# Performance work log

Hardware: AMD Instinct MI355X
Metric: run time of the kernel (lower is better)

## Reference

```python
import jax, jax.numpy as jnp
import numpy as np

P_FACTOR = 3.0
EPS = 1e-12  # torch F.normalize eps


def _l2norm(x):
    # torch.nn.functional.normalize(x, dim=1): x / max(||x||_2, eps)
    n = jnp.sqrt(jnp.sum(x * x, axis=1, keepdims=True))
    return x / jnp.maximum(n, EPS)


def setup_inputs() -> dict:
    key = jax.random.key(0)
    k1, k2, k3, k4, k5 = jax.random.split(key, 5)
    B, N, D_IN, D_RED, C = 8192, 16384, 1024, 512, 28
    return {
        "features": jax.random.normal(k1, (B, D_IN), dtype=jnp.float32),
        "ex_features": jax.random.normal(k2, (N, D_IN), dtype=jnp.float32),
        "g_w": jax.random.normal(k3, (D_RED, D_IN), dtype=jnp.float32) * 0.02,
        "g_b": jax.random.normal(k4, (D_RED,), dtype=jnp.float32) * 0.02,
        "ex_classes": jax.random.uniform(k5, (N, C), dtype=jnp.float32),
    }


def reference(features, ex_features, g_w, g_b, ex_classes):
    # g: Linear(input_dim -> dim_reduce)
    f = features @ g_w.T + g_b          # [B, D_red]
    ef = ex_features @ g_w.T + g_b      # [N, D_red]
    # cosine similarity
    s = _l2norm(f) @ _l2norm(ef).T      # [B, N]
    # power-sign activation: |s|^p * sign(s)
    a = jnp.power(jnp.abs(s), P_FACTOR) * jnp.sign(s)
    echo = a @ ex_classes               # [B, C]
    b = jnp.clip(jnp.sum(ex_classes, axis=0), 1.0, None)
    echo = jnp.clip(echo / b, 0.0, 1.0)
    return echo
```

## Files before the change

kernel.cpp:

```cpp
#include <hip/hip_runtime.h>
#include <stdint.h>

typedef __attribute__((ext_vector_type(4))) float f32x4;
typedef __attribute__((ext_vector_type(8))) short s16x8;

#define MFMA16(A, B, C) __builtin_amdgcn_mfma_f32_16x16x32_bf16(A, B, C, 0, 0, 0)
#define WAIT_VM(N) asm volatile("s_waitcnt vmcnt(" #N ")" ::: "memory")
#define WAIT_LGKM() asm volatile("s_waitcnt lgkmcnt(0)" ::: "memory")
#define BAR() __builtin_amdgcn_s_barrier()
#define SCHED_FENCE() __builtin_amdgcn_sched_barrier(0)
#define SP1() __builtin_amdgcn_s_setprio(1)
#define SP0() __builtin_amdgcn_s_setprio(0)

__device__ __forceinline__ unsigned short f2bf(float x) {
  union { float f; unsigned u; } v; v.f = x;
  return (unsigned short)((v.u + 0x7fffu + ((v.u >> 16) & 1u)) >> 16);
}

__global__ void k_cast_bf16(const float* __restrict__ in, unsigned short* __restrict__ out, int n4) {
  int i = blockIdx.x * blockDim.x + threadIdx.x;
  const int stride = gridDim.x * blockDim.x;
  for (; i < n4; i += stride) {
    const float4 v = ((const float4*)in)[i];
    ushort4 o;
    o.x = f2bf(v.x); o.y = f2bf(v.y); o.z = f2bf(v.z); o.w = f2bf(v.w);
    ((ushort4*)out)[i] = o;
  }
}

__global__ void k_excT(const float* __restrict__ exc, unsigned short* __restrict__ excT,
                       float* __restrict__ bvec) {
  const int c = blockIdx.x;
  const int tid = threadIdx.x;
  float sum = 0.f;
  for (int j = tid; j < 16384; j += 256) {
    const float v = (c < 28) ? exc[(size_t)j * 28 + c] : 0.f;
    excT[(size_t)c * 16384 + j] = f2bf(v);
    sum += v;
  }
  #pragma unroll
  for (int o = 32; o; o >>= 1) sum += __shfl_down(sum, o, 64);
  __shared__ float wsum[4];
  if ((tid & 63) == 0) wsum[tid >> 6] = sum;
  __syncthreads();
  if (tid == 0 && c < 28) bvec[c] = fmaxf(wsum[0] + wsum[1] + wsum[2] + wsum[3], 1.0f);
}

__device__ __forceinline__ void stage_a(const unsigned short* __restrict__ src, int ld,
                                        unsigned short* smem, int dsoff, int w, int offsrc) {
  #pragma unroll
  for (int c = 0; c < 4; ++c)
    __builtin_amdgcn_global_load_lds(
        (const __attribute__((address_space(1))) unsigned int*)(src + offsrc + c * 64 * ld),
        (__attribute__((address_space(3))) unsigned int*)(smem + dsoff + c * 4096 + w * 512),
        16, 0, 0);
}
__device__ __forceinline__ void stage_b(const unsigned short* __restrict__ src, int ld,
                                        unsigned short* smem, int dsoff, int w, int offsrc) {
  #pragma unroll
  for (int c = 0; c < 2; ++c)
    __builtin_amdgcn_global_load_lds(
        (const __attribute__((address_space(1))) unsigned int*)(src + offsrc + c * 64 * ld),
        (__attribute__((address_space(3))) unsigned int*)(smem + dsoff + c * 4096 + w * 512),
        16, 0, 0);
}

__device__ __forceinline__ void mma_step_p(const unsigned short* smem, int ao, int bo,
                                           int wr, int wc, int r, int q, f32x4 acc[8][2]) {
  const int rx = r & 7;
  #pragma unroll
  for (int ks = 0; ks < 2; ++ks) {
    const int sb = ((ks * 4 + q) ^ rx) << 3;
    s16x8 bf[2];
    #pragma unroll
    for (int j = 0; j < 2; ++j)
      bf[j] = *(const s16x8*)(smem + bo + (wc * 32 + j * 16 + r) * 64 + sb);
    #pragma unroll
    for (int i = 0; i < 8; ++i) {
      const s16x8 af = *(const s16x8*)(smem + ao + (wr * 128 + i * 16 + r) * 64 + sb);
      #pragma unroll
      for (int j = 0; j < 2; ++j)
        acc[i][j] = MFMA16(af, bf[j], acc[i][j]);
    }
  }
}

#define PA0 0
#define PB0 16384
#define PA1 24576
#define PB1 40960

__global__ __launch_bounds__(512, 2) void k_proj(const unsigned short* __restrict__ featbf,
                                                 const unsigned short* __restrict__ exbf,
                                                 const unsigned short* __restrict__ gwbf,
                                                 const float* __restrict__ gb,
                                                 float* __restrict__ fall) {
  __shared__ __align__(16) unsigned short smem[49152];
  const int tid = threadIdx.x, w = tid >> 6, lane = tid & 63;
  const int wr = w >> 2, wc = w & 3, r = lane & 15, q = lane >> 4;
  const int offsrc = (w * 8 + (lane >> 3)) * 1024 + (((lane & 7) ^ (lane >> 3)) << 3);
  const int m0 = blockIdx.x * 256;
  const int n0 = blockIdx.y * 128;
  const unsigned short* Asrc = (m0 < 8192) ? (featbf + (size_t)m0 * 1024)
                                           : (exbf + (size_t)(m0 - 8192) * 1024);
  const unsigned short* Bsrc = gwbf + (size_t)n0 * 1024;
  f32x4 acc[8][2];
  #pragma unroll
  for (int i = 0; i < 8; ++i)
    #pragma unroll
    for (int j = 0; j < 2; ++j) acc[i][j] = {0.f, 0.f, 0.f, 0.f};

  stage_a(Asrc, 1024, smem, PA0, w, offsrc);
  stage_b(Bsrc, 1024, smem, PB0, w, offsrc);
  for (int t = 0; t < 15; ++t) {
    const int na = ((t + 1) & 1) ? PA1 : PA0, nbb = ((t + 1) & 1) ? PB1 : PB0;
    stage_a(Asrc + (t + 1) * 64, 1024, smem, na, w, offsrc);
    stage_b(Bsrc + (t + 1) * 64, 1024, smem, nbb, w, offsrc);
    WAIT_VM(6);
    BAR();
    mma_step_p(smem, (t & 1) ? PA1 : PA0, (t & 1) ? PB1 : PB0, wr, wc, r, q, acc);
    WAIT_LGKM();
    BAR();
  }
  WAIT_VM(0);
  BAR();
  mma_step_p(smem, PA1, PB1, wr, wc, r, q, acc);

  #pragma unroll
  for (int j = 0; j < 2; ++j) {
    const int col = n0 + wc * 32 + j * 16 + r;
    const float bias = gb[col];
    #pragma unroll
    for (int i = 0; i < 8; ++i) {
      const int row0 = m0 + wr * 128 + i * 16 + q * 4;
      #pragma unroll
      for (int t = 0; t < 4; ++t)
        fall[(size_t)(row0 + t) * 512 + col] = acc[i][j][t] + bias;
    }
  }
}

__global__ __launch_bounds__(256) void k_norm(const float* __restrict__ fall,
                                              unsigned short* __restrict__ fn) {
  const int row = blockIdx.x * 4 + (threadIdx.x >> 6);
  const int lane = threadIdx.x & 63;
  const float4* p = (const float4*)(fall + (size_t)row * 512) + lane * 2;
  const float4 v0 = p[0], v1 = p[1];
  float ss = v0.x * v0.x + v0.y * v0.y + v0.z * v0.z + v0.w * v0.w
           + v1.x * v1.x + v1.y * v1.y + v1.z * v1.z + v1.w * v1.w;
  #pragma unroll
  for (int o = 32; o; o >>= 1) ss += __shfl_xor(ss, o, 64);
  const float sc = 1.0f / fmaxf(sqrtf(ss), 1e-12f);
  ushort4 o0, o1;
  o0.x = f2bf(v0.x * sc); o0.y = f2bf(v0.y * sc); o0.z = f2bf(v0.z * sc); o0.w = f2bf(v0.w * sc);
  o1.x = f2bf(v1.x * sc); o1.y = f2bf(v1.y * sc); o1.z = f2bf(v1.z * sc); o1.w = f2bf(v1.w * sc);
  ushort4* qo = (ushort4*)(fn + (size_t)row * 512) + lane * 2;
  qo[0] = o0; qo[1] = o1;
}

#define BUF 16384
#define EXLo 32768
#define ALo 40960

__device__ __forceinline__ void stage_p(const unsigned short* __restrict__ src,
                                        unsigned short* smem, int dsoff, int tid) {
  const int row = tid >> 2;
  const int scb = (tid & 3) ^ ((tid >> 3) & 3);
  const unsigned short* g = src + (size_t)row * 512 + scb * 8;
  __builtin_amdgcn_global_load_lds(
      (const __attribute__((address_space(1))) unsigned int*)g,
      (__attribute__((address_space(3))) unsigned int*)(smem + dsoff + tid * 8), 16, 0, 0);
}

__device__ __forceinline__ void stage_exc(const unsigned short* __restrict__ excTg, int c0,
                                          unsigned short* smem, int tid) {
  const int row = tid >> 5, b = tid & 31;
  const int sb = ((b & 24) | ((b ^ (row & 7)) & 7)) << 3;
  const unsigned short* g = excTg + (size_t)row * 16384 + c0 + sb;
  __builtin_amdgcn_global_load_lds(
      (const __attribute__((address_space(1))) unsigned int*)g,
      (__attribute__((address_space(3))) unsigned int*)(smem + EXLo + tid * 8), 16, 0, 0);
  __builtin_amdgcn_global_load_lds(
      (const __attribute__((address_space(1))) unsigned int*)(g + 16 * 16384),
      (__attribute__((address_space(3))) unsigned int*)(smem + EXLo + 4096 + tid * 8), 16, 0, 0);
}

__device__ __forceinline__ void ktile32(const unsigned short* smem, int bufR,
                                        int wr, int wc, int r, int q, int koff,
                                        f32x4 acc[2][2][4][2]) {
  const unsigned short* Bb = smem + bufR + 8192 + (wc * 32 + r) * 32 + koff;
  s16x8 bf[2][2];
  #pragma unroll
  for (int nh = 0; nh < 2; ++nh)
    #pragma unroll
    for (int fj = 0; fj < 2; ++fj)
      bf[nh][fj] = *(const s16x8*)(Bb + (nh * 128 + fj * 16) * 32);
  #pragma unroll
  for (int MH = 0; MH < 2; ++MH) {
    const unsigned short* Ab = smem + bufR + (MH * 128 + wr * 64 + r) * 32 + koff;
    #pragma unroll
    for (int fi = 0; fi < 4; ++fi) {
      const s16x8 af = *(const s16x8*)(Ab + fi * 512);
      #pragma unroll
      for (int nh = 0; nh < 2; ++nh)
        #pragma unroll
        for (int fj = 0; fj < 2; ++fj)
          acc[MH][nh][fi][fj] = MFMA16(af, bf[nh][fj], acc[MH][nh][fi][fj]);
    }
  }
}

__global__ __launch_bounds__(512, 2) void k_fused(const unsigned short* __restrict__ fnall,
                                                  const unsigned short* __restrict__ excT,
                                                  float* __restrict__ partial) {
  __shared__ __align__(16) unsigned short smem[73728];
  const int tid = threadIdx.x, w = tid >> 6, lane = tid & 63;
  const int wr = w >> 2, wc = w & 3, r = lane & 15, q = lane >> 4, rx = r & 7;
  const int koff = (q ^ ((r >> 1) & 3)) << 3;
  const int r0 = blockIdx.x * 256;
  const int nchunk = blockIdx.y;
  const unsigned short* Abase = fnall + (size_t)r0 * 512;
  const unsigned short* Ebase = fnall + (size_t)8192 * 512;
  unsigned short* aLb = smem + ALo;

  f32x4 acc[2][2][4][2];
  f32x4 eacc[2][2];
  #pragma unroll
  for (int a = 0; a < 2; ++a)
    #pragma unroll
    for (int b = 0; b < 2; ++b) eacc[a][b] = {0.f, 0.f, 0.f, 0.f};

  {
    const unsigned short* Bp = Ebase + (size_t)(nchunk * 4) * 256 * 512;
    stage_p(Bp, smem, 8192, tid);
    stage_p(Bp + 128 * 512, smem, 12288, tid);
    stage_p(Abase, smem, 0, tid);
    stage_p(Abase + 128 * 512, smem, 4096, tid);
  }

  for (int jt = 0; jt < 4; ++jt) {
    const int c0 = (nchunk * 4 + jt) * 256;
    const unsigned short* Bsrc = Ebase + (size_t)c0 * 512;
    #pragma unroll
    for (int a = 0; a < 2; ++a)
      #pragma unroll
      for (int b = 0; b < 2; ++b)
        #pragma unroll
        for (int fi = 0; fi < 4; ++fi)
          #pragma unroll
          for (int fj = 0; fj < 2; ++fj) acc[a][b][fi][fj] = {0.f, 0.f, 0.f, 0.f};

    for (int tk = 0; tk < 16; ++tk) {
      const int bufR = (tk & 1) * BUF, bufW = bufR ^ BUF;
      SCHED_FENCE(); WAIT_LGKM(); WAIT_VM(0); BAR(); SCHED_FENCE();
      if (tk < 15) {
        const unsigned short* An = Abase + (tk + 1) * 32;
        const unsigned short* Bn = Bsrc + (tk + 1) * 32;
        stage_p(Bn, smem, bufW + 8192, tid);
        stage_p(Bn + 128 * 512, smem, bufW + 12288, tid);
        stage_p(An, smem, bufW + 0, tid);
        stage_p(An + 128 * 512, smem, bufW + 4096, tid);
      } else {
        stage_exc(excT, c0, smem, tid);
        if (jt < 3) {
          const unsigned short* Bn = Ebase + (size_t)(c0 + 256) * 512;
          stage_p(Bn, smem, bufW + 8192, tid);
          stage_p(Bn + 128 * 512, smem, bufW + 12288, tid);
          stage_p(Abase, smem, bufW + 0, tid);
          stage_p(Abase + 128 * 512, smem, bufW + 4096, tid);
        }
      }
      SP1(); ktile32(smem, bufR, wr, wc, r, q, koff, acc); SP0();
    }

    SCHED_FENCE(); WAIT_LGKM();
    if (jt < 3) { WAIT_VM(4); } else { WAIT_VM(0); }
    BAR(); SCHED_FENCE();
    #pragma unroll
    for (int h = 0; h < 2; ++h) {
      #pragma unroll
      for (int nh = 0; nh < 2; ++nh)
        #pragma unroll
        for (int fi = 0; fi < 4; ++fi)
          #pragma unroll
          for (int fj = 0; fj < 2; ++fj) {
            const int colc = nh * 128 + wc * 32 + fj * 16 + r;
            const int cb = colc >> 3, cl = colc & 7;
            #pragma unroll
            for (int t2 = 0; t2 < 4; ++t2) {
              const int row = wr * 64 + fi * 16 + q * 4 + t2;
              const float v = acc[h][nh][fi][fj][t2];
              aLb[row * 256 + ((((cb & 24) | ((cb ^ (row & 7)) & 7)) << 3) | cl)] = f2bf(v * v * v);
            }
          }
      SCHED_FENCE(); WAIT_LGKM(); BAR(); SCHED_FENCE();
      {
        const int rE = w * 16 + r;
        const int re8 = rE & 7;
        #pragma unroll
        for (int kc = 0; kc < 8; ++kc) {
          const int kb = kc * 4 + q;
          const s16x8 af = *(const s16x8*)(aLb + rE * 256 + (((kb & 24) | ((kb ^ re8) & 7)) << 3));
          #pragma unroll
          for (int nj = 0; nj < 2; ++nj) {
            const s16x8 bfr = *(const s16x8*)(smem + EXLo + (nj * 16 + r) * 256 +
                                              (((kb & 24) | ((kb ^ rx) & 7)) << 3));
            eacc[h][nj] = MFMA16(af, bfr, eacc[h][nj]);
          }
        }
      }
      SCHED_FENCE(); WAIT_LGKM(); BAR(); SCHED_FENCE();
    }
  }

  #pragma unroll
  for (int h = 0; h < 2; ++h)
    #pragma unroll
    for (int nj = 0; nj < 2; ++nj) {
      const int rb = r0 + h * 128 + w * 16 + q * 4;
      const int cls = nj * 16 + r;
      #pragma unroll
      for (int t = 0; t < 4; ++t)
        partial[((size_t)nchunk * 8192 + rb + t) * 32 + cls] = eacc[h][nj][t];
    }
}

__global__ void k_reduce(const float* __restrict__ partial, const float* __restrict__ bvec,
                         float* __restrict__ out) {
  const int idx = blockIdx.x * 256 + threadIdx.x;
  const int row = idx / 28, c = idx - row * 28;
  float s = 0.f;
  #pragma unroll
  for (int nc = 0; nc < 16; ++nc) s += partial[((size_t)nc * 8192 + row) * 32 + c];
  out[idx] = fminf(fmaxf(s / bvec[c], 0.f), 1.f);
}

extern "C" void kernel_launch(void* const* d_in, const int* in_sizes, int n_in,
                              void* d_out, int out_size, void* d_ws, size_t ws_size,
                              hipStream_t stream) {
  const float* features    = (const float*)d_in[0];
  const float* ex_features = (const float*)d_in[1];
  const float* g_w         = (const float*)d_in[2];
  const float* g_b         = (const float*)d_in[3];
  const float* ex_classes  = (const float*)d_in[4];
  float* out = (float*)d_out;
  char* ws = (char*)d_ws;

  unsigned short* featbf = (unsigned short*)(ws + 0);
  unsigned short* exbf   = (unsigned short*)(ws + 16777216);
  unsigned short* fnall  = (unsigned short*)(ws + 0);
  float* fall            = (float*)(ws + 50331648);
  float* partial         = (float*)(ws + 50331648);
  unsigned short* gwbf   = (unsigned short*)(ws + 100663296);
  unsigned short* excT   = (unsigned short*)(ws + 101711872);
  float* bvec            = (float*)(ws + 102760448);

  k_cast_bf16<<<2048, 256, 0, stream>>>(features, featbf, 8192 * 1024 / 4);
  k_cast_bf16<<<2048, 256, 0, stream>>>(ex_features, exbf, 16384 * 1024 / 4);
  k_cast_bf16<<<512, 256, 0, stream>>>(g_w, gwbf, 512 * 1024 / 4);
  k_excT<<<32, 256, 0, stream>>>(ex_classes, excT, bvec);
  k_proj<<<dim3(96, 4), 512, 0, stream>>>(featbf, exbf, gwbf, g_b, fall);
  k_norm<<<6144, 256, 0, stream>>>(fall, fnall);
  k_fused<<<dim3(32, 16), 512, 0, stream>>>(fnall, excT, partial);
  k_reduce<<<896, 256, 0, stream>>>(partial, bvec, out);
}
```

Baseline: 245.2 us.

## Restructure K-loop sync to overlap LDS fragment reads with global prefetch

Inlines the per-k-tile MFMA routine and moves the barrier and vmcnt wait from the top of each iteration to the bottom. Each tile's LDS fragment reads are now issued before the next tile's global-to-LDS prefetch, and the second M-half's A fragments are loaded after the first half's MFMAs. The aim is to overlap LDS reads with async global loads and to shorten the stall before compute. The trade-off is more scattered wait and barrier placement, with some risk of a race on the double buffer and the exclass staging region.

```diff
diff --git a/kernel.cpp b/kernel.cpp
--- a/kernel.cpp
+++ b/kernel.cpp
@@ -185,31 +185,6 @@
       (__attribute__((address_space(3))) unsigned int*)(smem + EXLo + 4096 + tid * 8), 16, 0, 0);
 }
 
-__device__ __forceinline__ void ktile32(const unsigned short* smem, int bufR,
-                                        int wr, int wc, int r, int q, int koff,
-                                        f32x4 acc[2][2][4][2]) {
-  const unsigned short* Bb = smem + bufR + 8192 + (wc * 32 + r) * 32 + koff;
-  s16x8 bf[2][2];
-  #pragma unroll
-  for (int nh = 0; nh < 2; ++nh)
-    #pragma unroll
-    for (int fj = 0; fj < 2; ++fj)
-      bf[nh][fj] = *(const s16x8*)(Bb + (nh * 128 + fj * 16) * 32);
-  #pragma unroll
-  for (int MH = 0; MH < 2; ++MH) {
-    const unsigned short* Ab = smem + bufR + (MH * 128 + wr * 64 + r) * 32 + koff;
-    #pragma unroll
-    for (int fi = 0; fi < 4; ++fi) {
-      const s16x8 af = *(const s16x8*)(Ab + fi * 512);
-      #pragma unroll
-      for (int nh = 0; nh < 2; ++nh)
-        #pragma unroll
-        for (int fj = 0; fj < 2; ++fj)
-          acc[MH][nh][fi][fj] = MFMA16(af, bf[nh][fj], acc[MH][nh][fi][fj]);
-    }
-  }
-}
-
 __global__ __launch_bounds__(512, 2) void k_fused(const unsigned short* __restrict__ fnall,
                                                   const unsigned short* __restrict__ excT,
                                                   float* __restrict__ partial) {
@@ -236,6 +211,8 @@
     stage_p(Bp + 128 * 512, smem, 12288, tid);
     stage_p(Abase, smem, 0, tid);
     stage_p(Abase + 128 * 512, smem, 4096, tid);
+    WAIT_VM(0);
+    BAR(); SCHED_FENCE();
   }
 
   for (int jt = 0; jt < 4; ++jt) {
@@ -252,7 +229,19 @@
 
     for (int tk = 0; tk < 16; ++tk) {
       const int bufR = (tk & 1) * BUF, bufW = bufR ^ BUF;
-      SCHED_FENCE(); WAIT_LGKM(); WAIT_VM(0); BAR(); SCHED_FENCE();
+      s16x8 bf[2][2], af[4];
+      {
+        const unsigned short* Bb = smem + bufR + 8192 + (wc * 32 + r) * 32 + koff;
+        #pragma unroll
+        for (int nh = 0; nh < 2; ++nh)
+          #pragma unroll
+          for (int fj = 0; fj < 2; ++fj)
+            bf[nh][fj] = *(const s16x8*)(Bb + (nh * 128 + fj * 16) * 32);
+        const unsigned short* Ab0 = smem + bufR + (wr * 64 + r) * 32 + koff;
+        #pragma unroll
+        for (int fi = 0; fi < 4; ++fi)
+          af[fi] = *(const s16x8*)(Ab0 + fi * 512);
+      }
       if (tk < 15) {
         const unsigned short* An = Abase + (tk + 1) * 32;
         const unsigned short* Bn = Bsrc + (tk + 1) * 32;
@@ -270,12 +259,41 @@
           stage_p(Abase + 128 * 512, smem, bufW + 4096, tid);
         }
       }
-      SP1(); ktile32(smem, bufR, wr, wc, r, q, koff, acc); SP0();
-    }
-
-    SCHED_FENCE(); WAIT_LGKM();
-    if (jt < 3) { WAIT_VM(4); } else { WAIT_VM(0); }
-    BAR(); SCHED_FENCE();
+      SCHED_FENCE();
+      BAR();
+      WAIT_LGKM(); SCHED_FENCE();
+      SP1();
+      #pragma unroll
+      for (int fi = 0; fi < 4; ++fi)
+        #pragma unroll
+        for (int nh = 0; nh < 2; ++nh)
+          #pragma unroll
+          for (int fj = 0; fj < 2; ++fj)
+            acc[0][nh][fi][fj] = MFMA16(af[fi], bf[nh][fj], acc[0][nh][fi][fj]);
+      SP0();
+      {
+        const unsigned short* Ab1 = smem + bufR + ((128 + wr * 64 + r) * 32) + koff;
+        #pragma unroll
+        for (int fi = 0; fi < 4; ++fi)
+          af[fi] = *(const s16x8*)(Ab1 + fi * 512);
+      }
+      WAIT_LGKM(); SCHED_FENCE();
+      SP1();
+      #pragma unroll
+      for (int fi = 0; fi < 4; ++fi)
+        #pragma unroll
+        for (int nh = 0; nh < 2; ++nh)
+          #pragma unroll
+          for (int fj = 0; fj < 2; ++fj)
+            acc[1][nh][fi][fj] = MFMA16(af[fi], bf[nh][fj], acc[1][nh][fi][fj]);
+      SP0();
+      SCHED_FENCE();
+      if (tk < 15) { WAIT_VM(0); }
+      else if (jt < 3) { WAIT_VM(4); }
+      else { WAIT_VM(0); }
+      BAR(); SCHED_FENCE();
+    }
+
     #pragma unroll
     for (int h = 0; h < 2; ++h) {
       #pragma unroll
@@ -309,7 +327,9 @@
           }
         }
       }
-      SCHED_FENCE(); WAIT_LGKM(); BAR(); SCHED_FENCE();
+      SCHED_FENCE(); WAIT_LGKM();
+      if (h == 1) { WAIT_VM(0); }
+      BAR(); SCHED_FENCE();
     }
   }
 
```

New measurement: 250.6 us. 2.2% more time.

## Triple-buffer k-tile staging and split echo epilogue into quarter-row passes

Applied to the files above, without the earlier changes.

Replaces the double-buffered LDS staging for the similarity GEMM with a three-slot ring that prefetches two k-tiles ahead. The wait now leaves the most recent loads in flight (vmcnt 4/6) rather than draining everything each iteration. To fit the extra buffer in LDS, the cubed-similarity staging area for the echo GEMM shrinks to 64 rows. The epilogue therefore runs four passes in which half the waves write while all waves each do one MFMA chain. This adds barriers and some idle waves in the epilogue, and the larger LDS footprint could limit occupancy.

```diff
diff --git a/kernel.cpp b/kernel.cpp
--- a/kernel.cpp
+++ b/kernel.cpp
@@ -158,9 +158,8 @@
   qo[0] = o0; qo[1] = o1;
 }
 
-#define BUF 16384
-#define EXLo 32768
-#define ALo 40960
+#define EXLo 49152
+#define ALo 57344
 
 __device__ __forceinline__ void stage_p(const unsigned short* __restrict__ src,
                                         unsigned short* smem, int dsoff, int tid) {
@@ -170,6 +169,15 @@
   __builtin_amdgcn_global_load_lds(
       (const __attribute__((address_space(1))) unsigned int*)g,
       (__attribute__((address_space(3))) unsigned int*)(smem + dsoff + tid * 8), 16, 0, 0);
+}
+
+__device__ __forceinline__ void stage4(const unsigned short* __restrict__ A,
+                                       const unsigned short* __restrict__ B,
+                                       unsigned short* smem, int bufW, int tid) {
+  stage_p(B, smem, bufW + 8192, tid);
+  stage_p(B + 128 * 512, smem, bufW + 12288, tid);
+  stage_p(A, smem, bufW + 0, tid);
+  stage_p(A + 128 * 512, smem, bufW + 4096, tid);
 }
 
 __device__ __forceinline__ void stage_exc(const unsigned short* __restrict__ excTg, int c0,
@@ -224,23 +232,22 @@
   unsigned short* aLb = smem + ALo;
 
   f32x4 acc[2][2][4][2];
-  f32x4 eacc[2][2];
-  #pragma unroll
-  for (int a = 0; a < 2; ++a)
-    #pragma unroll
-    for (int b = 0; b < 2; ++b) eacc[a][b] = {0.f, 0.f, 0.f, 0.f};
+  f32x4 eacc4[4];
+  #pragma unroll
+  for (int a = 0; a < 4; ++a) eacc4[a] = {0.f, 0.f, 0.f, 0.f};
 
   {
-    const unsigned short* Bp = Ebase + (size_t)(nchunk * 4) * 256 * 512;
-    stage_p(Bp, smem, 8192, tid);
-    stage_p(Bp + 128 * 512, smem, 12288, tid);
-    stage_p(Abase, smem, 0, tid);
-    stage_p(Abase + 128 * 512, smem, 4096, tid);
+    const unsigned short* B0 = Ebase + (size_t)(nchunk * 4) * 256 * 512;
+    stage4(Abase, B0, smem, 0, tid);
+    SCHED_FENCE();
+    stage4(Abase + 32, B0 + 32, smem, 16384, tid);
+    SCHED_FENCE();
+    WAIT_VM(4);
+    BAR(); SCHED_FENCE();
   }
 
   for (int jt = 0; jt < 4; ++jt) {
     const int c0 = (nchunk * 4 + jt) * 256;
-    const unsigned short* Bsrc = Ebase + (size_t)c0 * 512;
     #pragma unroll
     for (int a = 0; a < 2; ++a)
       #pragma unroll
@@ -251,62 +258,67 @@
           for (int fj = 0; fj < 2; ++fj) acc[a][b][fi][fj] = {0.f, 0.f, 0.f, 0.f};
 
     for (int tk = 0; tk < 16; ++tk) {
-      const int bufR = (tk & 1) * BUF, bufW = bufR ^ BUF;
-      SCHED_FENCE(); WAIT_LGKM(); WAIT_VM(0); BAR(); SCHED_FENCE();
-      if (tk < 15) {
-        const unsigned short* An = Abase + (tk + 1) * 32;
-        const unsigned short* Bn = Bsrc + (tk + 1) * 32;
-        stage_p(Bn, smem, bufW + 8192, tid);
-        stage_p(Bn + 128 * 512, smem, bufW + 12288, tid);
-        stage_p(An, smem, bufW + 0, tid);
-        stage_p(An + 128 * 512, smem, bufW + 4096, tid);
-      } else {
+      const int g = jt * 16 + tk;
+      const int bufR = (g % 3) * 16384;
+      const int bufW = ((g + 2) % 3) * 16384;
+      if (tk == 15) {
         stage_exc(excT, c0, smem, tid);
-        if (jt < 3) {
-          const unsigned short* Bn = Ebase + (size_t)(c0 + 256) * 512;
-          stage_p(Bn, smem, bufW + 8192, tid);
-          stage_p(Bn + 128 * 512, smem, bufW + 12288, tid);
-          stage_p(Abase, smem, bufW + 0, tid);
-          stage_p(Abase + 128 * 512, smem, bufW + 4096, tid);
+        SCHED_FENCE();
+        if (g < 63) {
+          const int gn = g + 2;
+          stage4(Abase + (gn & 15) * 32,
+                 Ebase + (size_t)((nchunk * 4 + (gn >> 4)) * 256) * 512 + (gn & 15) * 32,
+                 smem, bufW, tid);
         }
+      } else if (g <= 61) {
+        const int gn = g + 2;
+        stage4(Abase + (gn & 15) * 32,
+               Ebase + (size_t)((nchunk * 4 + (gn >> 4)) * 256) * 512 + (gn & 15) * 32,
+               smem, bufW, tid);
       }
       SP1(); ktile32(smem, bufR, wr, wc, r, q, koff, acc); SP0();
-    }
-
-    SCHED_FENCE(); WAIT_LGKM();
+      SCHED_FENCE(); WAIT_LGKM();
+      if (tk == 15) { if (g < 63) { WAIT_VM(6); } }
+      else if (g == 62) { WAIT_VM(0); }
+      else { WAIT_VM(4); }
+      BAR(); SCHED_FENCE();
+    }
+
+    SCHED_FENCE();
     if (jt < 3) { WAIT_VM(4); } else { WAIT_VM(0); }
     BAR(); SCHED_FENCE();
     #pragma unroll
-    for (int h = 0; h < 2; ++h) {
-      #pragma unroll
-      for (int nh = 0; nh < 2; ++nh)
+    for (int h2 = 0; h2 < 4; ++h2) {
+      const int MHe = h2 >> 1;
+      if (wr == (h2 & 1)) {
         #pragma unroll
-        for (int fi = 0; fi < 4; ++fi)
+        for (int nh = 0; nh < 2; ++nh)
           #pragma unroll
-          for (int fj = 0; fj < 2; ++fj) {
-            const int colc = nh * 128 + wc * 32 + fj * 16 + r;
-            const int cb = colc >> 3, cl = colc & 7;
+          for (int fi = 0; fi < 4; ++fi)
             #pragma unroll
-            for (int t2 = 0; t2 < 4; ++t2) {
-              const int row = wr * 64 + fi * 16 + q * 4 + t2;
-              const float v = acc[h][nh][fi][fj][t2];
-              aLb[row * 256 + ((((cb & 24) | ((cb ^ (row & 7)) & 7)) << 3) | cl)] = f2bf(v * v * v);
+            for (int fj = 0; fj < 2; ++fj) {
+              const int colc = nh * 128 + wc * 32 + fj * 16 + r;
+              const int cb = colc >> 3, cl = colc & 7;
+              #pragma unroll
+              for (int t2 = 0; t2 < 4; ++t2) {
+                const int rowl = fi * 16 + q * 4 + t2;
+                const float v = acc[MHe][nh][fi][fj][t2];
+                aLb[rowl * 256 + ((((cb & 24) | ((cb ^ (rowl & 7)) & 7)) << 3) | cl)] = f2bf(v * v * v);
+              }
             }
-          }
+      }
       SCHED_FENCE(); WAIT_LGKM(); BAR(); SCHED_FENCE();
       {
-        const int rE = w * 16 + r;
-        const int re8 = rE & 7;
+        const int rEl = (w & 3) * 16 + r;
+        const int re8 = rEl & 7;
+        const int njo = (w >> 2) * 16;
         #pragma unroll
         for (int kc = 0; kc < 8; ++kc) {
           const int kb = kc * 4 + q;
-          const s16x8 af = *(const s16x8*)(aLb + rE * 256 + (((kb & 24) | ((kb ^ re8) & 7)) << 3));
-          #pragma unroll
-          for (int nj = 0; nj < 2; ++nj) {
-            const s16x8 bfr = *(const s16x8*)(smem + EXLo + (nj * 16 + r) * 256 +
-                                              (((kb & 24) | ((kb ^ rx) & 7)) << 3));
-            eacc[h][nj] = MFMA16(af, bfr, eacc[h][nj]);
-          }
+          const s16x8 af = *(const s16x8*)(aLb + rEl * 256 + (((kb & 24) | ((kb ^ re8) & 7)) << 3));
+          const s16x8 bfr = *(const s16x8*)(smem + EXLo + (njo + r) * 256 +
+                                            (((kb & 24) | ((kb ^ rx) & 7)) << 3));
+          eacc4[h2] = MFMA16(af, bfr, eacc4[h2]);
         }
       }
       SCHED_FENCE(); WAIT_LGKM(); BAR(); SCHED_FENCE();
@@ -314,15 +326,13 @@
   }
 
   #pragma unroll
-  for (int h = 0; h < 2; ++h)
-    #pragma unroll
-    for (int nj = 0; nj < 2; ++nj) {
-      const int rb = r0 + h * 128 + w * 16 + q * 4;
-      const int cls = nj * 16 + r;
-      #pragma unroll
-      for (int t = 0; t < 4; ++t)
-        partial[((size_t)nchunk * 8192 + rb + t) * 32 + cls] = eacc[h][nj][t];
-    }
+  for (int h2 = 0; h2 < 4; ++h2) {
+    const int rb = r0 + h2 * 64 + (w & 3) * 16 + q * 4;
+    const int cls = (w >> 2) * 16 + r;
+    #pragma unroll
+    for (int t = 0; t < 4; ++t)
+      partial[((size_t)nchunk * 8192 + rb + t) * 32 + cls] = eacc4[h2][t];
+  }
 }
 
 __global__ void k_reduce(const float* __restrict__ partial, const float* __restrict__ bvec,
```

Result: slower. 404.7 us (+65.0%).
